# Kernel optimization log

Hardware: AMD Instinct MI355X
Metric: run time of the kernel (lower is better)

Reference implementation:

```python
import jax, jax.numpy as jnp
import numpy as np

N, T, H, W, C = 4, 8, 64, 64, 512
WS = 8  # window size; H, W are exact multiples so pad/depad are identity


def setup_inputs() -> dict:
    key = jax.random.key(0)
    k1, k2, k3, k4 = jax.random.split(key, 4)
    x = jax.random.normal(k1, (N, T, H, W, C), dtype=jnp.float32)
    local_pos_embed = jax.random.normal(k2, (WS, WS, C), dtype=jnp.float32)
    W_in = jax.random.normal(k3, (3 * C, C), dtype=jnp.float32) * 0.02
    b_in = jnp.zeros((3 * C,), dtype=jnp.float32)
    W_out = jax.random.normal(k4, (C, C), dtype=jnp.float32) * 0.02
    b_out = jnp.zeros((C,), dtype=jnp.float32)
    return {"x": x, "local_pos_embed": local_pos_embed, "W_in": W_in,
            "b_in": b_in, "W_out": W_out, "b_out": b_out, "num_heads": 8}


def reference(x, local_pos_embed, W_in, b_in, W_out, b_out, num_heads):
    n, t, h, w, c = x.shape
    ws = local_pos_embed.shape[0]
    nh, nw = h // ws, w // ws
    head_dim = c // num_heads
    scale = 1.0 / jnp.sqrt(jnp.asarray(head_dim, dtype=x.dtype))

    # window partition: (N*T, H, W, C) -> (N*T*nh*nw, ws*ws, C)
    xw = x.reshape(n * t, nh, ws, nw, ws, c)
    xw = xw.transpose(0, 1, 3, 2, 4, 5).reshape(n * t * nh * nw, ws * ws, c)

    pos = local_pos_embed.reshape(ws * ws, c)  # flatten(0,1)
    qk_in = xw + pos[None, :, :]               # pos added to q,k only

    Wq, Wk, Wv = W_in[:c], W_in[c:2 * c], W_in[2 * c:]
    bq, bk, bv = b_in[:c], b_in[c:2 * c], b_in[2 * c:]

    B, S = qk_in.shape[0], qk_in.shape[1]
    q = (qk_in @ Wq.T + bq).reshape(B, S, num_heads, head_dim)
    k = (qk_in @ Wk.T + bk).reshape(B, S, num_heads, head_dim)
    v = (xw @ Wv.T + bv).reshape(B, S, num_heads, head_dim)

    scores = jnp.einsum('bqhd,bkhd->bhqk', q * scale, k)
    attn = jax.nn.softmax(scores, axis=-1)
    out = jnp.einsum('bhqk,bkhd->bqhd', attn, v).reshape(B, S, c)
    out = out @ W_out.T + b_out

    # reverse window partition
    out = out.reshape(n * t, nh, nw, ws, ws, c)
    out = out.transpose(0, 1, 3, 2, 4, 5).reshape(n, t, h, w, c)
    return out
```

## Files before the change

kernel.cpp:

```cpp
#include <hip/hip_runtime.h>

typedef _Float16 f16;
typedef unsigned int u32;
typedef f16 f16x8 __attribute__((ext_vector_type(8)));
typedef f16 f16x4 __attribute__((ext_vector_type(4)));
typedef float f32x4 __attribute__((ext_vector_type(4)));


__device__ __forceinline__ int src_row(int m) {
    int win = m >> 6, s = m & 63;
    return ((win >> 6) << 12) | (((win >> 3) & 7) << 9) | ((s >> 3) << 6) |
           ((win & 7) << 3) | (s & 7);
}

__device__ __forceinline__ void gload_lds16(const void* g, void* lds) {
    __builtin_amdgcn_global_load_lds(
        (const __attribute__((address_space(1))) u32*)g,
        (__attribute__((address_space(3))) u32*)lds, 16, 0, 0);
}

__device__ __forceinline__ f16* sp(char* S, int r, int c) {
    return (f16*)(S + r * 1024 + ((c * 2) ^ ((r & 7) << 4)));
}

__global__ __launch_bounds__(256) void prep_weights_k(
        const float* __restrict__ Wi, const float* __restrict__ Wo,
        f16* __restrict__ Wi_h, f16* __restrict__ Wo_h) {
    int i = blockIdx.x * 256 + threadIdx.x;
    const float4* src;
    f16* dst;
    int idx;
    if (i < 196608) { src = (const float4*)Wi; dst = Wi_h; idx = i; }
    else            { src = (const float4*)Wo; dst = Wo_h; idx = i - 196608; }
    float4 v = src[idx];
    f16x4 h = {(f16)v.x, (f16)v.y, (f16)v.z, (f16)v.w};
    *(f16x4*)(dst + (size_t)idx * 4) = h;
}

__global__ __launch_bounds__(256) void prep_bias_k(
        const float* __restrict__ pos, const float* __restrict__ Wi,
        const float* __restrict__ b_in, float* __restrict__ biasT) {
    int idx = blockIdx.x * 256 + threadIdx.x;
    int s = idx / 1536, o = idx % 1536;
    float acc = b_in[o];
    if (o < 1024) {
        const float4* p4 = (const float4*)(pos + (size_t)s * 512);
        const float4* w4 = (const float4*)(Wi + (size_t)o * 512);
        #pragma unroll 4
        for (int c = 0; c < 128; ++c) {
            float4 a = p4[c], b = w4[c];
            acc += a.x * b.x + a.y * b.y + a.z * b.z + a.w * b.w;
        }
    }
    biasT[idx] = acc;
}

__global__ __launch_bounds__(256) void prep_x_k(
        const float* __restrict__ x, f16* __restrict__ xh, int m0) {
    int i = blockIdx.x * 256 + threadIdx.x;
    int ml = i >> 6, c8 = (i & 63) * 8;
    int sr = src_row(m0 + ml);
    const float4* s4 = (const float4*)(x + (size_t)sr * 512 + c8);
    float4 a = s4[0], b = s4[1];
    f16x8 hv = {(f16)a.x, (f16)a.y, (f16)a.z, (f16)a.w,
                (f16)b.x, (f16)b.y, (f16)b.z, (f16)b.w};
    *(f16x8*)(xh + (size_t)ml * 512 + c8) = hv;
}

__global__ __launch_bounds__(256) void qkv_gemm_k(
        const f16* __restrict__ xh, const f16* __restrict__ Wh,
        const float* __restrict__ biasT, f16* __restrict__ qkv, int nblk) {
    __shared__ f16 As[128 * 32];
    __shared__ f16 Bs[128 * 32];
    int tid = threadIdx.x;
    int lane = tid & 63, wid = tid >> 6;
    int l15 = lane & 15, g = lane >> 4;
    int sid = (blockIdx.x & 7) * (nblk >> 3) + (blockIdx.x >> 3);
    int bn = sid % 12, bm = sid / 12;
    int brow = bm * 128, bcol = bn * 128;
    int wm = wid >> 1, wn = wid & 1;
    int brB = lane >> 2, bcB = (lane & 3) * 8;

    const f16* Abase = xh + (size_t)brow * 512;
    const f16* Bbase = Wh + (size_t)bcol * 512;

    f32x4 zero4 = {0.f, 0.f, 0.f, 0.f};
    f32x4 acc[4][4];
    #pragma unroll
    for (int a = 0; a < 4; ++a)
        #pragma unroll
        for (int b = 0; b < 4; ++b) acc[a][b] = zero4;

    for (int kt = 0; kt < 16; ++kt) {
        int k0 = kt * 32;
        #pragma unroll
        for (int i = 0; i < 2; ++i) {
            int chunk = wid * 2 + i;
            gload_lds16(Abase + (size_t)(chunk * 16 + brB) * 512 + k0 + bcB,
                        (void*)&As[chunk * 512]);
            gload_lds16(Bbase + (size_t)(chunk * 16 + brB) * 512 + k0 + bcB,
                        (void*)&Bs[chunk * 512]);
        }
        __syncthreads();
        f16x8 af[4], bfr[4];
        #pragma unroll
        for (int mf = 0; mf < 4; ++mf)
            af[mf] = *reinterpret_cast<const f16x8*>(&As[(wm * 64 + mf * 16 + l15) * 32 + g * 8]);
        #pragma unroll
        for (int nf = 0; nf < 4; ++nf)
            bfr[nf] = *reinterpret_cast<const f16x8*>(&Bs[(wn * 64 + nf * 16 + l15) * 32 + g * 8]);
        #pragma unroll
        for (int mf = 0; mf < 4; ++mf)
            #pragma unroll
            for (int nf = 0; nf < 4; ++nf)
                acc[mf][nf] = __builtin_amdgcn_mfma_f32_16x16x32_f16(af[mf], bfr[nf], acc[mf][nf], 0, 0, 0);
        __syncthreads();
    }

    #pragma unroll
    for (int mf = 0; mf < 4; ++mf) {
        #pragma unroll
        for (int nf = 0; nf < 4; ++nf) {
            int col = bcol + wn * 64 + nf * 16 + l15;
            #pragma unroll
            for (int j = 0; j < 4; ++j) {
                int rowl = brow + wm * 64 + mf * 16 + g * 4 + j;
                float v = acc[mf][nf][j] + biasT[(rowl & 63) * 1536 + col];
                qkv[(size_t)rowl * 1536 + col] = (f16)v;
            }
        }
    }
}

__global__ __launch_bounds__(512) void attn_out_k(
        const f16* __restrict__ qkv, const f16* __restrict__ Woh,
        const float* __restrict__ b_out, float* __restrict__ out, int w0) {
    __shared__ __align__(16) char S[64 * 1024];
    int tid = threadIdx.x;
    int lane = tid & 63, h = tid >> 6;
    int l15 = lane & 15, g = lane >> 4;
    const f16* base = qkv + (size_t)blockIdx.x * 64 * 1536;
    int qc = h * 64, kc = 512 + h * 64, vc = 1024 + h * 64;

    f32x4 zero4 = {0.f, 0.f, 0.f, 0.f};
    f32x4 acc[4][4];
    #pragma unroll
    for (int a = 0; a < 4; ++a)
        #pragma unroll
        for (int b = 0; b < 4; ++b) acc[a][b] = zero4;

    {
        f16x8 qf[4][2], kf[4][2];
        #pragma unroll
        for (int mf = 0; mf < 4; ++mf)
            #pragma unroll
            for (int ks = 0; ks < 2; ++ks)
                qf[mf][ks] = *reinterpret_cast<const f16x8*>(base + (size_t)(mf * 16 + l15) * 1536 + qc + ks * 32 + g * 8);
        #pragma unroll
        for (int nf = 0; nf < 4; ++nf)
            #pragma unroll
            for (int ks = 0; ks < 2; ++ks)
                kf[nf][ks] = *reinterpret_cast<const f16x8*>(base + (size_t)(nf * 16 + l15) * 1536 + kc + ks * 32 + g * 8);
        #pragma unroll
        for (int ks = 0; ks < 2; ++ks)
            #pragma unroll
            for (int mf = 0; mf < 4; ++mf)
                #pragma unroll
                for (int nf = 0; nf < 4; ++nf)
                    acc[mf][nf] = __builtin_amdgcn_mfma_f32_16x16x32_f16(qf[mf][ks], kf[nf][ks], acc[mf][nf], 0, 0, 0);
    }

    f16x8 vf[4][2];
    #pragma unroll
    for (int nf = 0; nf < 4; ++nf)
        #pragma unroll
        for (int ks = 0; ks < 2; ++ks) {
            f16x8 v;
            #pragma unroll
            for (int j = 0; j < 8; ++j)
                v[j] = base[(size_t)(ks * 32 + g * 8 + j) * 1536 + vc + nf * 16 + l15];
            vf[nf][ks] = v;
        }

    #pragma unroll
    for (int mf = 0; mf < 4; ++mf) {
        #pragma unroll
        for (int j = 0; j < 4; ++j) {
            float mx = -1e30f;
            #pragma unroll
            for (int nf = 0; nf < 4; ++nf) mx = fmaxf(mx, acc[mf][nf][j]);
            #pragma unroll
            for (int off = 1; off < 16; off <<= 1) mx = fmaxf(mx, __shfl_xor(mx, off));
            float e[4], sum = 0.f;
            #pragma unroll
            for (int nf = 0; nf < 4; ++nf) {
                e[nf] = __expf((acc[mf][nf][j] - mx) * 0.125f);
                sum += e[nf];
            }
            #pragma unroll
            for (int off = 1; off < 16; off <<= 1) sum += __shfl_xor(sum, off);
            float rinv = __fdividef(1.0f, sum);
            int row = mf * 16 + g * 4 + j;
            #pragma unroll
            for (int nf = 0; nf < 4; ++nf)
                *sp(S, row, h * 64 + nf * 16 + l15) = (f16)(e[nf] * rinv);
        }
    }

    f32x4 acc2[4][4];
    #pragma unroll
    for (int a = 0; a < 4; ++a)
        #pragma unroll
        for (int b = 0; b < 4; ++b) acc2[a][b] = zero4;
    #pragma unroll
    for (int ks = 0; ks < 2; ++ks)
        #pragma unroll
        for (int mf = 0; mf < 4; ++mf) {
            f16x8 pa = *reinterpret_cast<const f16x8*>(sp(S, mf * 16 + l15, h * 64 + ks * 32 + g * 8));
            #pragma unroll
            for (int nf = 0; nf < 4; ++nf)
                acc2[mf][nf] = __builtin_amdgcn_mfma_f32_16x16x32_f16(pa, vf[nf][ks], acc2[mf][nf], 0, 0, 0);
        }
    #pragma unroll
    for (int mf = 0; mf < 4; ++mf)
        #pragma unroll
        for (int nf = 0; nf < 4; ++nf)
            #pragma unroll
            for (int j = 0; j < 4; ++j)
                *sp(S, mf * 16 + g * 4 + j, h * 64 + nf * 16 + l15) = (f16)acc2[mf][nf][j];

    __syncthreads();

    int ocol0 = h * 64;
    float bo[4];
    #pragma unroll
    for (int nf = 0; nf < 4; ++nf) bo[nf] = b_out[ocol0 + nf * 16 + l15];

    #pragma unroll
    for (int a = 0; a < 4; ++a)
        #pragma unroll
        for (int b = 0; b < 4; ++b) acc[a][b] = zero4;
    for (int ks = 0; ks < 16; ++ks) {
        f16x8 af[4], bf[4];
        #pragma unroll
        for (int mf = 0; mf < 4; ++mf)
            af[mf] = *reinterpret_cast<const f16x8*>(sp(S, mf * 16 + l15, ks * 32 + g * 8));
        #pragma unroll
        for (int nf = 0; nf < 4; ++nf)
            bf[nf] = *reinterpret_cast<const f16x8*>(Woh + (size_t)(ocol0 + nf * 16 + l15) * 512 + ks * 32 + g * 8);
        #pragma unroll
        for (int mf = 0; mf < 4; ++mf)
            #pragma unroll
            for (int nf = 0; nf < 4; ++nf)
                acc[mf][nf] = __builtin_amdgcn_mfma_f32_16x16x32_f16(af[mf], bf[nf], acc[mf][nf], 0, 0, 0);
    }

    int wglob = w0 + blockIdx.x;
    #pragma unroll
    for (int mf = 0; mf < 4; ++mf) {
        #pragma unroll
        for (int j = 0; j < 4; ++j) {
            int srow = src_row(wglob * 64 + mf * 16 + g * 4 + j);
            #pragma unroll
            for (int nf = 0; nf < 4; ++nf)
                out[(size_t)srow * 512 + ocol0 + nf * 16 + l15] = acc[mf][nf][j] + bo[nf];
        }
    }
}

extern "C" void kernel_launch(void* const* d_in, const int* in_sizes, int n_in,
                              void* d_out, int out_size, void* d_ws, size_t ws_size,
                              hipStream_t stream) {
    (void)in_sizes; (void)n_in; (void)out_size;
    const float* x     = (const float*)d_in[0];
    const float* pos   = (const float*)d_in[1];
    const float* W_in  = (const float*)d_in[2];
    const float* b_in  = (const float*)d_in[3];
    const float* W_out = (const float*)d_in[4];
    const float* b_out = (const float*)d_in[5];
    float* out = (float*)d_out;

    char* ws = (char*)d_ws;
    f16*   Wi_h  = (f16*)ws;
    f16*   Wo_h  = (f16*)(ws + 1572864);
    float* biasT = (float*)(ws + 2097152);
    const size_t fixed = 2490368;

    int chunks = 4;
    while (chunks < 64) {
        size_t need = fixed + ((size_t)131072 / chunks) * 4096;
        if (need <= ws_size) break;
        chunks <<= 1;
    }
    int Mc = 131072 / chunks;
    f16* xh  = (f16*)(ws + fixed);
    f16* qkv = (f16*)(ws + fixed + (size_t)Mc * 1024);
    int nblk = (Mc / 128) * 12;

    prep_weights_k<<<1024, 256, 0, stream>>>(W_in, W_out, Wi_h, Wo_h);
    prep_bias_k<<<384, 256, 0, stream>>>(pos, W_in, b_in, biasT);
    for (int c = 0; c < chunks; ++c) {
        int m0 = c * Mc;
        prep_x_k<<<Mc / 4, 256, 0, stream>>>(x, xh, m0);
        qkv_gemm_k<<<nblk, 256, 0, stream>>>(xh, Wi_h, biasT, qkv, nblk);
        attn_out_k<<<Mc / 64, 512, 0, stream>>>(qkv, Wo_h, b_out, out, c * (Mc / 64));
    }
}
```

Baseline: 707.6 us.

## Rewrite QKV GEMM as 256x256 tile, 8-wave, double-buffered pipelined kernel

Replaces the 128x128, 4-wave QKV projection GEMM with a 256x256-tile, 512-thread kernel using 128 KB of dynamic LDS. The K=512 reduction runs in 64-wide steps with double buffering, XOR-swizzled LDS layout, and async global-to-LDS loads that are interleaved with MFMA work, plus fine-grained barriers and s_setprio. The goal is higher data reuse per tile, fewer LDS bank conflicts, and overlap of load latency with compute. The cost is much higher LDS and register use per block, which limits occupancy, and fewer blocks per chunk, which may underfill the GPU's compute units.

```diff
diff --git a/kernel.cpp b/kernel.cpp
--- a/kernel.cpp
+++ b/kernel.cpp
@@ -67,66 +67,106 @@
     *(f16x8*)(xh + (size_t)ml * 512 + c8) = hv;
 }
 
-__global__ __launch_bounds__(256) void qkv_gemm_k(
+__global__ void __launch_bounds__(512, 2) qkv_gemm8_k(
         const f16* __restrict__ xh, const f16* __restrict__ Wh,
         const float* __restrict__ biasT, f16* __restrict__ qkv, int nblk) {
-    __shared__ f16 As[128 * 32];
-    __shared__ f16 Bs[128 * 32];
+    extern __shared__ f16 lds[];
     int tid = threadIdx.x;
     int lane = tid & 63, wid = tid >> 6;
     int l15 = lane & 15, g = lane >> 4;
+    int wm = wid >> 2, wn = wid & 3;
     int sid = (blockIdx.x & 7) * (nblk >> 3) + (blockIdx.x >> 3);
-    int bn = sid % 12, bm = sid / 12;
-    int brow = bm * 128, bcol = bn * 128;
-    int wm = wid >> 1, wn = wid & 1;
-    int brB = lane >> 2, bcB = (lane & 3) * 8;
-
-    const f16* Abase = xh + (size_t)brow * 512;
-    const f16* Bbase = Wh + (size_t)bcol * 512;
-
+    int bm = sid / 6, bn = sid % 6;
+    const f16* Ap = xh + (size_t)bm * 256 * 512;
+    const f16* Bp = Wh + (size_t)bn * 256 * 512;
+
+    int li0 = tid, li1 = tid + 512;
+    int r0 = li0 >> 3, c0 = li0 & 7, r1 = li1 >> 3, c1 = li1 & 7;
+    int off0 = r0 * 512 + ((c0 ^ (r0 & 7)) * 8);
+    int off1 = r1 * 512 + ((c1 ^ (r1 & 7)) * 8);
+
+    auto stage = [&](const f16* panel, int ldsbase, int tt, int h) {
+        int tb = tt & 1;
+        int dst = ldsbase + (tb * 2 + h) * 8192 + wid * 512;
+        const f16* src = panel + h * 65536 + tt * 64;
+        gload_lds16(src + off0, (void*)&lds[dst]);
+        gload_lds16(src + off1, (void*)&lds[dst + 4096]);
+    };
+
+    f32x4 acc[8][4];
     f32x4 zero4 = {0.f, 0.f, 0.f, 0.f};
-    f32x4 acc[4][4];
-    #pragma unroll
-    for (int a = 0; a < 4; ++a)
+    #pragma unroll
+    for (int a = 0; a < 8; ++a)
         #pragma unroll
         for (int b = 0; b < 4; ++b) acc[a][b] = zero4;
-
-    for (int kt = 0; kt < 16; ++kt) {
-        int k0 = kt * 32;
-        #pragma unroll
-        for (int i = 0; i < 2; ++i) {
-            int chunk = wid * 2 + i;
-            gload_lds16(Abase + (size_t)(chunk * 16 + brB) * 512 + k0 + bcB,
-                        (void*)&As[chunk * 512]);
-            gload_lds16(Bbase + (size_t)(chunk * 16 + brB) * 512 + k0 + bcB,
-                        (void*)&Bs[chunk * 512]);
-        }
-        __syncthreads();
-        f16x8 af[4], bfr[4];
-        #pragma unroll
-        for (int mf = 0; mf < 4; ++mf)
-            af[mf] = *reinterpret_cast<const f16x8*>(&As[(wm * 64 + mf * 16 + l15) * 32 + g * 8]);
-        #pragma unroll
-        for (int nf = 0; nf < 4; ++nf)
-            bfr[nf] = *reinterpret_cast<const f16x8*>(&Bs[(wn * 64 + nf * 16 + l15) * 32 + g * 8]);
-        #pragma unroll
-        for (int mf = 0; mf < 4; ++mf)
-            #pragma unroll
-            for (int nf = 0; nf < 4; ++nf)
-                acc[mf][nf] = __builtin_amdgcn_mfma_f32_16x16x32_f16(af[mf], bfr[nf], acc[mf][nf], 0, 0, 0);
-        __syncthreads();
-    }
-
-    #pragma unroll
-    for (int mf = 0; mf < 4; ++mf) {
+    f16x8 bf[4][2];
+
+    stage(Ap, 0, 0, 0); stage(Ap, 0, 0, 1);
+    stage(Bp, 32768, 0, 0); stage(Bp, 32768, 0, 1);
+    stage(Ap, 0, 1, 0); stage(Ap, 0, 1, 1);
+    stage(Bp, 32768, 1, 0); stage(Bp, 32768, 1, 1);
+    asm volatile("s_waitcnt vmcnt(0)" ::: "memory");
+    __builtin_amdgcn_s_barrier();
+
+    #pragma unroll
+    for (int tt = 0; tt < 8; ++tt) {
+        int tb = tt & 1;
+        const f16* Ab = &lds[(tb * 2 + wm) * 8192];
+        const f16* Bb = &lds[32768 + (tb * 2 + (wn >> 1)) * 8192];
+        #pragma unroll
+        for (int q = 0; q < 4; ++q) {
+            f16x8 af[2][2];
+            #pragma unroll
+            for (int ml = 0; ml < 2; ++ml) {
+                int rr = (q * 2 + ml) * 16 + l15;
+                #pragma unroll
+                for (int ks = 0; ks < 2; ++ks)
+                    af[ml][ks] = *(const f16x8*)&Ab[rr * 64 + (((ks * 4 + g) ^ (rr & 7)) * 8)];
+            }
+            if (q == 0) {
+                #pragma unroll
+                for (int nf = 0; nf < 4; ++nf) {
+                    int rb = (wn & 1) * 64 + nf * 16 + l15;
+                    #pragma unroll
+                    for (int ks = 0; ks < 2; ++ks)
+                        bf[nf][ks] = *(const f16x8*)&Bb[rb * 64 + (((ks * 4 + g) ^ (rb & 7)) * 8)];
+                }
+            }
+            if (q <= 1) {
+                if ((tt & 1) ? (tt + 1 < 8) : (tt >= 2)) stage(Ap, 0, tt + 1, q);
+            } else {
+                if (tt + 2 < 8) stage(Bp, 32768, tt + 2, q - 2);
+            }
+            __builtin_amdgcn_s_barrier();
+            __builtin_amdgcn_s_setprio(1);
+            #pragma unroll
+            for (int ml = 0; ml < 2; ++ml)
+                #pragma unroll
+                for (int nf = 0; nf < 4; ++nf)
+                    #pragma unroll
+                    for (int ks = 0; ks < 2; ++ks)
+                        acc[q * 2 + ml][nf] = __builtin_amdgcn_mfma_f32_16x16x32_f16(
+                            af[ml][ks], bf[nf][ks], acc[q * 2 + ml][nf], 0, 0, 0);
+            __builtin_amdgcn_s_setprio(0);
+            if (q == 3) {
+                if (tt < 6)       asm volatile("s_waitcnt vmcnt(4)" ::: "memory");
+                else if (tt == 6) asm volatile("s_waitcnt vmcnt(0)" ::: "memory");
+            }
+            __builtin_amdgcn_s_barrier();
+        }
+    }
+
+    int browg = bm * 256 + wm * 128, bcolg = bn * 256 + wn * 64;
+    #pragma unroll
+    for (int mf = 0; mf < 8; ++mf) {
         #pragma unroll
         for (int nf = 0; nf < 4; ++nf) {
-            int col = bcol + wn * 64 + nf * 16 + l15;
+            int col = bcolg + nf * 16 + l15;
             #pragma unroll
             for (int j = 0; j < 4; ++j) {
-                int rowl = brow + wm * 64 + mf * 16 + g * 4 + j;
-                float v = acc[mf][nf][j] + biasT[(rowl & 63) * 1536 + col];
-                qkv[(size_t)rowl * 1536 + col] = (f16)v;
+                int row = browg + mf * 16 + g * 4 + j;
+                float v = acc[mf][nf][j] + biasT[(row & 63) * 1536 + col];
+                qkv[(size_t)row * 1536 + col] = (f16)v;
             }
         }
     }
@@ -295,14 +335,17 @@
     int Mc = 131072 / chunks;
     f16* xh  = (f16*)(ws + fixed);
     f16* qkv = (f16*)(ws + fixed + (size_t)Mc * 1024);
-    int nblk = (Mc / 128) * 12;
+    int nblk = (Mc / 256) * 6;
+
+    static_cast<void>(hipFuncSetAttribute((const void*)qkv_gemm8_k,
+        hipFuncAttributeMaxDynamicSharedMemorySize, 131072));
 
     prep_weights_k<<<1024, 256, 0, stream>>>(W_in, W_out, Wi_h, Wo_h);
     prep_bias_k<<<384, 256, 0, stream>>>(pos, W_in, b_in, biasT);
     for (int c = 0; c < chunks; ++c) {
         int m0 = c * Mc;
         prep_x_k<<<Mc / 4, 256, 0, stream>>>(x, xh, m0);
-        qkv_gemm_k<<<nblk, 256, 0, stream>>>(xh, Wi_h, biasT, qkv, nblk);
+        qkv_gemm8_k<<<nblk, 512, 131072, stream>>>(xh, Wi_h, biasT, qkv, nblk);
         attn_out_k<<<Mc / 64, 512, 0, stream>>>(qkv, Wo_h, b_out, out, c * (Mc / 64));
     }
 }
```

New measurement: 650.0 us. -8.1%, faster.
